# Performance work log

Hardware: AMD Instinct MI355X
Metric: run time of the kernel (lower is better)

Reference implementation:

```python
import jax, jax.numpy as jnp
import numpy as np

B = 1
F, Hh, Ww = 2, 30, 52           # grid_sizes (frames, height, width); 30*52 = 1560 tokens/frame
L = F * Hh * Ww                  # 3120 tokens
DIM = 1536
NH = 12
HD = DIM // NH                   # 128
EPS = 1e-6
SCALE = 1.0 / np.sqrt(HD)


def _rope_angles():
    # Matches causal_rope_apply: head_dim/2 = 64 complex channels split 22/21/21 (t/h/w).
    c = HD // 2
    tc = c - 2 * (c // 3)
    hc = c // 3
    wc = c // 3
    def ax(n, dh):
        inv = 1.0 / np.power(10000.0, np.arange(dh) * 2.0 / (2 * dh))
        return np.outer(np.arange(n), inv)  # [n, dh]
    ft, fh, fw = ax(F, tc), ax(Hh, hc), ax(Ww, wc)
    ang = np.concatenate([
        np.broadcast_to(ft[:, None, None, :], (F, Hh, Ww, tc)),
        np.broadcast_to(fh[None, :, None, :], (F, Hh, Ww, hc)),
        np.broadcast_to(fw[None, None, :, :], (F, Hh, Ww, wc)),
    ], axis=-1).reshape(L, c)
    return jnp.asarray(np.cos(ang), jnp.float32), jnp.asarray(np.sin(ang), jnp.float32)


def setup_inputs() -> dict:
    key = jax.random.key(0)
    ks = jax.random.split(key, 8)
    s = 1.0 / np.sqrt(DIM)
    d = {
        'x':  jax.random.normal(ks[0], (B, L, DIM), jnp.float32),
        'wq': jax.random.normal(ks[1], (DIM, DIM), jnp.float32) * s,
        'wk': jax.random.normal(ks[2], (DIM, DIM), jnp.float32) * s,
        'wv': jax.random.normal(ks[3], (DIM, DIM), jnp.float32) * s,
        'wo': jax.random.normal(ks[4], (DIM, DIM), jnp.float32) * s,
        'bq': jax.random.normal(ks[5], (DIM,), jnp.float32) * 0.02,
        'bk': jax.random.normal(ks[6], (DIM,), jnp.float32) * 0.02,
        'bv': jax.random.normal(ks[7], (DIM,), jnp.float32) * 0.02,
        'bo': jnp.zeros((DIM,), jnp.float32),
        'gq': jnp.ones((DIM,), jnp.float32),   # RMSNorm gain for q
        'gk': jnp.ones((DIM,), jnp.float32),   # RMSNorm gain for k
    }
    cos, sin = _rope_angles()
    d['freqs_cos'] = cos   # [L, HD//2]
    d['freqs_sin'] = sin
    return d


def _rms(x, g):
    return x * jax.lax.rsqrt(jnp.mean(x * x, axis=-1, keepdims=True) + EPS) * g


def _rope(x, cos, sin):
    # x: [B, L, NH, HD]; complex pairs are (even, odd) consecutive channels
    xs = x.reshape(B, L, NH, HD // 2, 2)
    xr, xi = xs[..., 0], xs[..., 1]
    c = cos[None, :, None, :]
    s = sin[None, :, None, :]
    out = jnp.stack([xr * c - xi * s, xr * s + xi * c], axis=-1)
    return out.reshape(B, L, NH, HD)


def reference(x, wq, wk, wv, wo, bq, bk, bv, bo, gq, gk, freqs_cos, freqs_sin):
    q = _rms(x @ wq + bq, gq).reshape(B, L, NH, HD)
    k = _rms(x @ wk + bk, gk).reshape(B, L, NH, HD)
    v = (x @ wv + bv).reshape(B, L, NH, HD)
    q = _rope(q, freqs_cos, freqs_sin)
    k = _rope(k, freqs_cos, freqs_sin)
    # block-causal per frame: query in frame i attends to keys in frames <= i
    frame = jnp.arange(L) // (Hh * Ww)
    mask = frame[None, :] <= frame[:, None]                     # [Lq, Lk]
    scores = jnp.einsum('bihd,bjhd->bhij', q, k) * SCALE        # [B, NH, L, L]
    scores = jnp.where(mask[None, None], scores, jnp.finfo(scores.dtype).min)
    p = jax.nn.softmax(scores, axis=-1)
    out = jnp.einsum('bhij,bjhd->bihd', p, v).reshape(B, L, DIM)
    return out @ wo + bo
```

## Files before the change

### kernel.cpp

```cpp
#include <hip/hip_runtime.h>
#include <hip/hip_bf16.h>

#define L_SEQ 3120
#define LPAD  3200
#define DIMN  1536
#define FRAME 1560
#define NHH   12
#define HDIM  128

using bh8   = __attribute__((ext_vector_type(8))) short;
using bh4   = __attribute__((ext_vector_type(4))) short;
using f32x4 = __attribute__((ext_vector_type(4))) float;
typedef unsigned short u16;
typedef unsigned int   u32;

static __device__ __forceinline__ u16 f2bf(float f) {
  __hip_bfloat16 h = __float2bfloat16(f);
  return *reinterpret_cast<u16*>(&h);
}
static __device__ __forceinline__ void gld16(const u16* g, u16* l) {
  __builtin_amdgcn_global_load_lds((const __attribute__((address_space(1))) void*)g,
                                   (__attribute__((address_space(3))) void*)l, 16, 0, 0);
}

__global__ __launch_bounds__(256) void prep_x_kern(const float* __restrict__ x,
                                                   u16* __restrict__ xb) {
  int i = (blockIdx.x * 256 + threadIdx.x) * 8;
  bh8 o;
  if (i < L_SEQ * DIMN) {
    float4 a = *(const float4*)&x[i];
    float4 b = *(const float4*)&x[i + 4];
    o[0] = (short)f2bf(a.x); o[1] = (short)f2bf(a.y);
    o[2] = (short)f2bf(a.z); o[3] = (short)f2bf(a.w);
    o[4] = (short)f2bf(b.x); o[5] = (short)f2bf(b.y);
    o[6] = (short)f2bf(b.z); o[7] = (short)f2bf(b.w);
  } else {
    o = (bh8){0, 0, 0, 0, 0, 0, 0, 0};
  }
  *(bh8*)&xb[i] = o;
}

__global__ __launch_bounds__(256) void transpose_w_kern(const float* __restrict__ w0, const float* __restrict__ w1,
                                 const float* __restrict__ w2, const float* __restrict__ w3,
                                 u16* __restrict__ t0, u16* __restrict__ t1,
                                 u16* __restrict__ t2, u16* __restrict__ t3) {
  __shared__ float tile[32][33];
  const float* src; u16* dst;
  switch (blockIdx.z) {
    case 0:  src = w0; dst = t0; break;
    case 1:  src = w1; dst = t1; break;
    case 2:  src = w2; dst = t2; break;
    default: src = w3; dst = t3; break;
  }
  int k0 = blockIdx.x * 32, n0 = blockIdx.y * 32;
  int tx = threadIdx.x, ty = threadIdx.y;
  #pragma unroll
  for (int i = 0; i < 4; i++)
    tile[ty * 4 + i][tx] = src[(size_t)(k0 + ty * 4 + i) * DIMN + n0 + tx];
  __syncthreads();
  #pragma unroll
  for (int i = 0; i < 4; i++) {
    int ry = ty * 4 + i;
    dst[(size_t)(n0 + ry) * DIMN + k0 + tx] = f2bf(tile[tx][ry]);
  }
}

__global__ __launch_bounds__(256) void zero_tail_kern(u16* __restrict__ ob) {
  int i = (blockIdx.x * 256 + threadIdx.x) * 8;
  *(bh8*)&ob[L_SEQ * DIMN + i] = (bh8){0, 0, 0, 0, 0, 0, 0, 0};
}

__global__ __launch_bounds__(256) void gemm_qkv(const u16* __restrict__ A,
                                                const u16* __restrict__ Bt,
                                                const float* __restrict__ bq,
                                                const float* __restrict__ bk,
                                                const float* __restrict__ bv,
                                                float* __restrict__ lin,
                                                u16* __restrict__ Vt) {
  __shared__ __align__(16) u16 Al[128 * 64];
  __shared__ __align__(16) u16 Bl[128 * 64];
  int t = threadIdx.x, lane = t & 63, w = t >> 6;
  int m0 = blockIdx.x * 128, n0 = blockIdx.y * 128;
  int wr = (w >> 1) * 64, wc = (w & 1) * 64;
  int r16 = lane & 15, g8 = (lane >> 4) * 8;
  int lrow = lane >> 3, lcol = (lane & 7) * 8;
  f32x4 acc[4][4];
  #pragma unroll
  for (int i = 0; i < 4; i++)
    #pragma unroll
    for (int j = 0; j < 4; j++) acc[i][j] = (f32x4){0.f, 0.f, 0.f, 0.f};

  const u16* Abase = A + (size_t)(m0 + w * 32 + lrow) * DIMN + lcol;
  const u16* Bbase = Bt + (size_t)(n0 + w * 32 + lrow) * DIMN + lcol;

  for (int kt = 0; kt < DIMN; kt += 64) {
    __syncthreads();
    #pragma unroll
    for (int j = 0; j < 4; j++) {
      gld16(Abase + (size_t)j * 8 * DIMN + kt, &Al[(w * 32 + j * 8) * 64]);
      gld16(Bbase + (size_t)j * 8 * DIMN + kt, &Bl[(w * 32 + j * 8) * 64]);
    }
    __syncthreads();
    bh8 af[2][4], bf[2][4];
    #pragma unroll
    for (int kk = 0; kk < 2; kk++) {
      #pragma unroll
      for (int i = 0; i < 4; i++)
        af[kk][i] = *(const bh8*)&Al[(wr + i * 16 + r16) * 64 + kk * 32 + g8];
      #pragma unroll
      for (int j = 0; j < 4; j++)
        bf[kk][j] = *(const bh8*)&Bl[(wc + j * 16 + r16) * 64 + kk * 32 + g8];
    }
    #pragma unroll
    for (int kk = 0; kk < 2; kk++)
      #pragma unroll
      for (int i = 0; i < 4; i++)
        #pragma unroll
        for (int j = 0; j < 4; j++)
          acc[i][j] = __builtin_amdgcn_mfma_f32_16x16x32_bf16(af[kk][i], bf[kk][j], acc[i][j], 0, 0, 0);
  }

  int cr = (lane >> 4) * 4, cc = lane & 15;
  int seg = n0 / DIMN;
  int nb0 = n0 - seg * DIMN;
  const float* bp = (seg == 0) ? bq : (seg == 1) ? bk : bv;
  if (seg < 2) {
    #pragma unroll
    for (int j = 0; j < 4; j++) {
      int n = nb0 + wc + j * 16 + cc;
      float bvv = bp[n];
      #pragma unroll
      for (int i = 0; i < 4; i++) {
        int m = m0 + wr + i * 16 + cr;
        float* orow = lin + (size_t)m * (2 * DIMN) + seg * DIMN + n;
        #pragma unroll
        for (int r = 0; r < 4; r++) orow[(size_t)r * (2 * DIMN)] = acc[i][j][r] + bvv;
      }
    }
  } else {
    #pragma unroll
    for (int j = 0; j < 4; j++) {
      int d = nb0 + wc + j * 16 + cc;
      float bvv = bp[d];
      #pragma unroll
      for (int i = 0; i < 4; i++) {
        int m = m0 + wr + i * 16 + cr;
        if (m < L_SEQ) {
          bh4 o;
          #pragma unroll
          for (int r = 0; r < 4; r++) o[r] = (short)f2bf(acc[i][j][r] + bvv);
          *(bh4*)&Vt[(size_t)d * L_SEQ + m] = o;
        }
      }
    }
  }
}

__global__ __launch_bounds__(256) void gemm_out(const u16* __restrict__ A,
                                                const u16* __restrict__ Bt,
                                                const float* __restrict__ bias,
                                                float* __restrict__ out) {
  __shared__ __align__(16) u16 Al[128 * 64];
  __shared__ __align__(16) u16 Bl[128 * 64];
  int t = threadIdx.x, lane = t & 63, w = t >> 6;
  int m0 = blockIdx.x * 128, n0 = blockIdx.y * 128;
  int wr = (w >> 1) * 64, wc = (w & 1) * 64;
  int r16 = lane & 15, g8 = (lane >> 4) * 8;
  int lrow = lane >> 3, lcol = (lane & 7) * 8;
  f32x4 acc[4][4];
  #pragma unroll
  for (int i = 0; i < 4; i++)
    #pragma unroll
    for (int j = 0; j < 4; j++) acc[i][j] = (f32x4){0.f, 0.f, 0.f, 0.f};

  const u16* Abase = A + (size_t)(m0 + w * 32 + lrow) * DIMN + lcol;
  const u16* Bbase = Bt + (size_t)(n0 + w * 32 + lrow) * DIMN + lcol;

  for (int kt = 0; kt < DIMN; kt += 64) {
    __syncthreads();
    #pragma unroll
    for (int j = 0; j < 4; j++) {
      gld16(Abase + (size_t)j * 8 * DIMN + kt, &Al[(w * 32 + j * 8) * 64]);
      gld16(Bbase + (size_t)j * 8 * DIMN + kt, &Bl[(w * 32 + j * 8) * 64]);
    }
    __syncthreads();
    bh8 af[2][4], bf[2][4];
    #pragma unroll
    for (int kk = 0; kk < 2; kk++) {
      #pragma unroll
      for (int i = 0; i < 4; i++)
        af[kk][i] = *(const bh8*)&Al[(wr + i * 16 + r16) * 64 + kk * 32 + g8];
      #pragma unroll
      for (int j = 0; j < 4; j++)
        bf[kk][j] = *(const bh8*)&Bl[(wc + j * 16 + r16) * 64 + kk * 32 + g8];
    }
    #pragma unroll
    for (int kk = 0; kk < 2; kk++)
      #pragma unroll
      for (int i = 0; i < 4; i++)
        #pragma unroll
        for (int j = 0; j < 4; j++)
          acc[i][j] = __builtin_amdgcn_mfma_f32_16x16x32_bf16(af[kk][i], bf[kk][j], acc[i][j], 0, 0, 0);
  }

  int cr = (lane >> 4) * 4, cc = lane & 15;
  #pragma unroll
  for (int j = 0; j < 4; j++) {
    int n = n0 + wc + j * 16 + cc;
    float bvv = bias[n];
    #pragma unroll
    for (int i = 0; i < 4; i++) {
      int m = m0 + wr + i * 16 + cr;
      if (m < L_SEQ) {
        #pragma unroll
        for (int r = 0; r < 4; r++) out[(size_t)(m + r) * DIMN + n] = acc[i][j][r] + bvv;
      }
    }
  }
}

__global__ __launch_bounds__(256) void postproc_qk(const float* __restrict__ lin,
                                                   const float* __restrict__ gq,
                                                   const float* __restrict__ gk,
                                                   const float* __restrict__ fc,
                                                   const float* __restrict__ fs,
                                                   u16* __restrict__ Qb, u16* __restrict__ Kb) {
  int l = blockIdx.x, t = threadIdx.x;
  int lane = t & 63, w = t >> 6;
  const float2* qr = (const float2*)(lin + (size_t)l * (2 * DIMN));
  const float2* kr = qr + DIMN / 2;
  float2 qv[3], kv[3];
  float ssq = 0.f, ssk = 0.f;
  #pragma unroll
  for (int j = 0; j < 3; j++) {
    qv[j] = qr[t + j * 256];
    kv[j] = kr[t + j * 256];
    ssq += qv[j].x * qv[j].x + qv[j].y * qv[j].y;
    ssk += kv[j].x * kv[j].x + kv[j].y * kv[j].y;
  }
  __shared__ float red[8];
  #pragma unroll
  for (int off = 32; off; off >>= 1) {
    ssq += __shfl_xor(ssq, off);
    ssk += __shfl_xor(ssk, off);
  }
  if (lane == 0) { red[w] = ssq; red[4 + w] = ssk; }
  __syncthreads();
  float rrq = rsqrtf((red[0] + red[1] + red[2] + red[3]) * (1.0f / DIMN) + 1e-6f);
  float rrk = rsqrtf((red[4] + red[5] + red[6] + red[7]) * (1.0f / DIMN) + 1e-6f);
  u32* qo = (u32*)Qb;
  u32* ko = (u32*)Kb;
  #pragma unroll
  for (int j = 0; j < 3; j++) {
    int p = t + j * 256;
    int head = p >> 6, c = p & 63;
    float co = fc[l * 64 + c], si = fs[l * 64 + c];
    float2 g2, o;
    size_t idx = ((size_t)head * L_SEQ + l) * 64 + c;
    g2 = ((const float2*)gq)[p];
    o.x = qv[j].x * rrq * g2.x; o.y = qv[j].y * rrq * g2.y;
    qo[idx] = (u32)f2bf(o.x * co - o.y * si) | ((u32)f2bf(o.x * si + o.y * co) << 16);
    g2 = ((const float2*)gk)[p];
    o.x = kv[j].x * rrk * g2.x; o.y = kv[j].y * rrk * g2.y;
    ko[idx] = (u32)f2bf(o.x * co - o.y * si) | ((u32)f2bf(o.x * si + o.y * co) << 16);
  }
}

__global__ __launch_bounds__(256) void attn_kern(const u16* __restrict__ Q,
                                                 const u16* __restrict__ K,
                                                 const u16* __restrict__ Vt,
                                                 u16* __restrict__ Ob) {
  __shared__ __align__(16) u16 KlB[2][64 * 128];
  __shared__ __align__(16) u16 VlB[2][128 * 64];
  __shared__ __align__(16) u16 Pl[4][16 * 72];
  int t = threadIdx.x, lane = t & 63, w = t >> 6;
  int h = blockIdx.y;
  int bx = 48 - blockIdx.x;
  int qb = bx * 64, qr0 = qb + w * 16;
  int r16 = lane & 15, grp = lane >> 4, g8 = grp * 8;
  int cr = grp * 4, cc = lane & 15;
  const float sl = 0.08838834764831845f * 1.4426950408889634f;

  int qld = qr0 + r16; if (qld > L_SEQ - 1) qld = L_SEQ - 1;
  const u16* qrow = Q + ((size_t)h * L_SEQ + qld) * HDIM;
  bh8 qf[4];
  #pragma unroll
  for (int kk = 0; kk < 4; kk++) qf[kk] = *(const bh8*)&qrow[kk * 32 + g8];

  const u16* Kbase = K + (size_t)h * L_SEQ * HDIM;
  const u16* Vbase = Vt + (size_t)h * HDIM * L_SEQ;

  float m_run[4] = {-3.0e38f, -3.0e38f, -3.0e38f, -3.0e38f};
  float l_part[4] = {0.f, 0.f, 0.f, 0.f};
  f32x4 accO[8];
  #pragma unroll
  for (int i = 0; i < 8; i++) accO[i] = (f32x4){0.f, 0.f, 0.f, 0.f};

  int klim_min = (qr0 < FRAME) ? FRAME : L_SEQ;
  int klimr[4];
  #pragma unroll
  for (int r = 0; r < 4; r++) klimr[r] = (qr0 + cr + r < FRAME) ? FRAME : L_SEQ;
  int klimB = (qb + 63 < FRAME) ? FRAME : L_SEQ;
  int nkt = (klimB + 63) >> 6;

  auto stage = [&](int buf, int it) {
    int kt = it << 6;
    #pragma unroll
    for (int j = 0; j < 4; j++) {
      int rr = w * 16 + j * 4 + (lane >> 4);
      int grow = kt + rr; grow = (grow > L_SEQ - 1) ? L_SEQ - 1 : grow;
      int gc = ((lane & 15) ^ (rr & 7)) * 8;
      gld16(Kbase + (size_t)grow * HDIM + gc, &KlB[buf][(w * 16 + j * 4) * 128]);
    }
    #pragma unroll
    for (int j = 0; j < 4; j++) {
      int vr = w * 32 + j * 8 + (lane >> 3);
      int gc = kt + ((lane & 7) ^ (vr & 7)) * 8;
      gc = (gc > L_SEQ - 8) ? L_SEQ - 8 : gc;
      gld16(Vbase + (size_t)vr * L_SEQ + gc, &VlB[buf][(w * 32 + j * 8) * 64]);
    }
  };

  stage(0, 0);
  for (int it = 0; it < nkt; ++it) {
    int buf = it & 1, kt = it << 6;
    if (it + 1 < nkt) {
      stage(buf ^ 1, it + 1);
      asm volatile("s_waitcnt vmcnt(8)" ::: "memory");
    } else {
      asm volatile("s_waitcnt vmcnt(0)" ::: "memory");
    }
    __builtin_amdgcn_s_barrier();
    __builtin_amdgcn_sched_barrier(0);

    f32x4 s[4];
    #pragma unroll
    for (int sb = 0; sb < 4; sb++) s[sb] = (f32x4){0.f, 0.f, 0.f, 0.f};
    #pragma unroll
    for (int kk = 0; kk < 4; kk++)
      #pragma unroll
      for (int sb = 0; sb < 4; sb++) {
        int rr = sb * 16 + r16;
        bh8 kf = *(const bh8*)&KlB[buf][rr * 128 + (((kk * 4 + grp) ^ (rr & 7)) * 8)];
        s[sb] = __builtin_amdgcn_mfma_f32_16x16x32_bf16(qf[kk], kf, s[sb], 0, 0, 0);
      }

    float v[4][4];
    if (kt + 64 > klim_min) {
      #pragma unroll
      for (int sb = 0; sb < 4; sb++) {
        int j = kt + sb * 16 + cc;
        #pragma unroll
        for (int r = 0; r < 4; r++) v[sb][r] = (j < klimr[r]) ? s[sb][r] * sl : -3.0e38f;
      }
    } else {
      #pragma unroll
      for (int sb = 0; sb < 4; sb++)
        #pragma unroll
        for (int r = 0; r < 4; r++) v[sb][r] = s[sb][r] * sl;
    }

    float loc[4];
    #pragma unroll
    for (int r = 0; r < 4; r++)
      loc[r] = fmaxf(fmaxf(v[0][r], v[1][r]), fmaxf(v[2][r], v[3][r]));
    bool need = (loc[0] > m_run[0] + 8.f) || (loc[1] > m_run[1] + 8.f) ||
                (loc[2] > m_run[2] + 8.f) || (loc[3] > m_run[3] + 8.f);
    if (__any((int)need)) {
      float facs[4];
      #pragma unroll
      for (int r = 0; r < 4; r++) {
        float mx = loc[r];
        mx = fmaxf(mx, __shfl_xor(mx, 1));
        mx = fmaxf(mx, __shfl_xor(mx, 2));
        mx = fmaxf(mx, __shfl_xor(mx, 4));
        mx = fmaxf(mx, __shfl_xor(mx, 8));
        float mnew = fmaxf(m_run[r], mx);
        facs[r] = exp2f(m_run[r] - mnew);
        m_run[r] = mnew;
        l_part[r] *= facs[r];
      }
      #pragma unroll
      for (int nb = 0; nb < 8; nb++)
        #pragma unroll
        for (int r = 0; r < 4; r++) accO[nb][r] *= facs[r];
    }
    #pragma unroll
    for (int sb = 0; sb < 4; sb++)
      #pragma unroll
      for (int r = 0; r < 4; r++) {
        float p = exp2f(v[sb][r] - m_run[r]);
        l_part[r] += p;
        Pl[w][(cr + r) * 72 + sb * 16 + cc] = f2bf(p);
      }

    bh8 pf0 = *(const bh8*)&Pl[w][r16 * 72 + g8];
    bh8 pf1 = *(const bh8*)&Pl[w][r16 * 72 + 32 + g8];
    #pragma unroll
    for (int nb = 0; nb < 8; nb++) {
      int vrow = nb * 16 + r16;
      bh8 vf0 = *(const bh8*)&VlB[buf][vrow * 64 + ((grp ^ (vrow & 7)) * 8)];
      bh8 vf1 = *(const bh8*)&VlB[buf][vrow * 64 + (((4 + grp) ^ (vrow & 7)) * 8)];
      accO[nb] = __builtin_amdgcn_mfma_f32_16x16x32_bf16(pf0, vf0, accO[nb], 0, 0, 0);
      accO[nb] = __builtin_amdgcn_mfma_f32_16x16x32_bf16(pf1, vf1, accO[nb], 0, 0, 0);
    }
    __builtin_amdgcn_s_barrier();
  }

  #pragma unroll
  for (int r = 0; r < 4; r++) {
    float lr = l_part[r];
    lr += __shfl_xor(lr, 1);
    lr += __shfl_xor(lr, 2);
    lr += __shfl_xor(lr, 4);
    lr += __shfl_xor(lr, 8);
    l_part[r] = 1.0f / lr;
  }
  #pragma unroll
  for (int nb = 0; nb < 8; nb++)
    #pragma unroll
    for (int r = 0; r < 4; r++) {
      int qi = qr0 + cr + r;
      if (qi < L_SEQ)
        Ob[(size_t)qi * DIMN + h * HDIM + nb * 16 + cc] = f2bf(accO[nb][r] * l_part[r]);
    }
}

extern "C" void kernel_launch(void* const* d_in, const int* in_sizes, int n_in,
                              void* d_out, int out_size, void* d_ws, size_t ws_size,
                              hipStream_t stream) {
  const float* x  = (const float*)d_in[0];
  const float* wq = (const float*)d_in[1];
  const float* wk = (const float*)d_in[2];
  const float* wv = (const float*)d_in[3];
  const float* wo = (const float*)d_in[4];
  const float* bq = (const float*)d_in[5];
  const float* bk = (const float*)d_in[6];
  const float* bv = (const float*)d_in[7];
  const float* bo = (const float*)d_in[8];
  const float* gq = (const float*)d_in[9];
  const float* gk = (const float*)d_in[10];
  const float* fc = (const float*)d_in[11];
  const float* fs = (const float*)d_in[12];

  char* ws = (char*)d_ws;
  u16* xb   = (u16*)(ws);
  u16* Btq  = (u16*)(ws + 9830400);
  u16* wot  = (u16*)(ws + 23986176);
  u16* Qb   = (u16*)(ws + 28704768);
  u16* Kb   = (u16*)(ws + 38289408);
  u16* Vt   = (u16*)(ws + 47874048);
  u16* Ob   = (u16*)(ws + 57458688);
  float* lin = (float*)(ws + 67289088);

  prep_x_kern<<<2400, 256, 0, stream>>>(x, xb);
  transpose_w_kern<<<dim3(48, 48, 4), dim3(32, 8), 0, stream>>>(
      wq, wk, wv, wo, Btq, Btq + DIMN * DIMN, Btq + 2 * DIMN * DIMN, wot);
  zero_tail_kern<<<60, 256, 0, stream>>>(Ob);

  gemm_qkv<<<dim3(25, 36), 256, 0, stream>>>(xb, Btq, bq, bk, bv, lin, Vt);
  postproc_qk<<<L_SEQ, 256, 0, stream>>>(lin, gq, gk, fc, fs, Qb, Kb);
  attn_kern<<<dim3(49, 12), 256, 0, stream>>>(Qb, Kb, Vt, Ob);
  gemm_out<<<dim3(25, 12), 256, 0, stream>>>(Ob, wot, bo, (float*)d_out);
}
```

Before: 398.2 us.

## Process two 16-row query slices per wave in attention to double K/V reuse

Each attention wave now handles 32 query rows (two 16-row slices), making the block tile 128 queries and halving the grid. Every K/V tile loaded into LDS and every K fragment read is reused for twice as many queries, reducing memory traffic and LDS reads per FLOP. Priority hints are added around the MFMA sections. The trade-off is higher register usage, lower occupancy and a smaller grid with coarser causal-tile granularity.

```diff
diff --git a/kernel.cpp b/kernel.cpp
--- a/kernel.cpp
+++ b/kernel.cpp
@@ -275,32 +275,42 @@
   __shared__ __align__(16) u16 Pl[4][16 * 72];
   int t = threadIdx.x, lane = t & 63, w = t >> 6;
   int h = blockIdx.y;
-  int bx = 48 - blockIdx.x;
-  int qb = bx * 64, qr0 = qb + w * 16;
+  int bx = 24 - blockIdx.x;
+  int qb = bx * 128, qr0 = qb + w * 32;
   int r16 = lane & 15, grp = lane >> 4, g8 = grp * 8;
   int cr = grp * 4, cc = lane & 15;
   const float sl = 0.08838834764831845f * 1.4426950408889634f;
 
-  int qld = qr0 + r16; if (qld > L_SEQ - 1) qld = L_SEQ - 1;
-  const u16* qrow = Q + ((size_t)h * L_SEQ + qld) * HDIM;
-  bh8 qf[4];
-  #pragma unroll
-  for (int kk = 0; kk < 4; kk++) qf[kk] = *(const bh8*)&qrow[kk * 32 + g8];
+  bh8 qf[2][4];
+  #pragma unroll
+  for (int qs = 0; qs < 2; qs++) {
+    int qld = qr0 + qs * 16 + r16; if (qld > L_SEQ - 1) qld = L_SEQ - 1;
+    const u16* qrow = Q + ((size_t)h * L_SEQ + qld) * HDIM;
+    #pragma unroll
+    for (int kk = 0; kk < 4; kk++) qf[qs][kk] = *(const bh8*)&qrow[kk * 32 + g8];
+  }
 
   const u16* Kbase = K + (size_t)h * L_SEQ * HDIM;
   const u16* Vbase = Vt + (size_t)h * HDIM * L_SEQ;
 
-  float m_run[4] = {-3.0e38f, -3.0e38f, -3.0e38f, -3.0e38f};
-  float l_part[4] = {0.f, 0.f, 0.f, 0.f};
-  f32x4 accO[8];
-  #pragma unroll
-  for (int i = 0; i < 8; i++) accO[i] = (f32x4){0.f, 0.f, 0.f, 0.f};
+  float m_run[2][4], l_part[2][4];
+  f32x4 accO[2][8];
+  #pragma unroll
+  for (int qs = 0; qs < 2; qs++) {
+    #pragma unroll
+    for (int r = 0; r < 4; r++) { m_run[qs][r] = -3.0e38f; l_part[qs][r] = 0.f; }
+    #pragma unroll
+    for (int i = 0; i < 8; i++) accO[qs][i] = (f32x4){0.f, 0.f, 0.f, 0.f};
+  }
 
   int klim_min = (qr0 < FRAME) ? FRAME : L_SEQ;
-  int klimr[4];
-  #pragma unroll
-  for (int r = 0; r < 4; r++) klimr[r] = (qr0 + cr + r < FRAME) ? FRAME : L_SEQ;
-  int klimB = (qb + 63 < FRAME) ? FRAME : L_SEQ;
+  int klimr[2][4];
+  #pragma unroll
+  for (int qs = 0; qs < 2; qs++)
+    #pragma unroll
+    for (int r = 0; r < 4; r++)
+      klimr[qs][r] = (qr0 + qs * 16 + cr + r < FRAME) ? FRAME : L_SEQ;
+  int klimB = (qb + 127 < FRAME) ? FRAME : L_SEQ;
   int nkt = (klimB + 63) >> 6;
 
   auto stage = [&](int buf, int it) {
@@ -333,97 +343,125 @@
     __builtin_amdgcn_s_barrier();
     __builtin_amdgcn_sched_barrier(0);
 
-    f32x4 s[4];
-    #pragma unroll
-    for (int sb = 0; sb < 4; sb++) s[sb] = (f32x4){0.f, 0.f, 0.f, 0.f};
-    #pragma unroll
-    for (int kk = 0; kk < 4; kk++)
-      #pragma unroll
-      for (int sb = 0; sb < 4; sb++) {
-        int rr = sb * 16 + r16;
-        bh8 kf = *(const bh8*)&KlB[buf][rr * 128 + (((kk * 4 + grp) ^ (rr & 7)) * 8)];
-        s[sb] = __builtin_amdgcn_mfma_f32_16x16x32_bf16(qf[kk], kf, s[sb], 0, 0, 0);
-      }
-
-    float v[4][4];
+    f32x4 s[2][4];
+    #pragma unroll
+    for (int qs = 0; qs < 2; qs++)
+      #pragma unroll
+      for (int sb = 0; sb < 4; sb++) s[qs][sb] = (f32x4){0.f, 0.f, 0.f, 0.f};
+    #pragma unroll
+    for (int sb = 0; sb < 4; sb++) {
+      int rr = sb * 16 + r16;
+      bh8 kf[4];
+      #pragma unroll
+      for (int kk = 0; kk < 4; kk++)
+        kf[kk] = *(const bh8*)&KlB[buf][rr * 128 + (((kk * 4 + grp) ^ (rr & 7)) * 8)];
+      __builtin_amdgcn_s_setprio(1);
+      #pragma unroll
+      for (int qs = 0; qs < 2; qs++)
+        #pragma unroll
+        for (int kk = 0; kk < 4; kk++)
+          s[qs][sb] = __builtin_amdgcn_mfma_f32_16x16x32_bf16(qf[qs][kk], kf[kk], s[qs][sb], 0, 0, 0);
+      __builtin_amdgcn_s_setprio(0);
+    }
+
+    float v[2][4][4];
     if (kt + 64 > klim_min) {
       #pragma unroll
-      for (int sb = 0; sb < 4; sb++) {
-        int j = kt + sb * 16 + cc;
-        #pragma unroll
-        for (int r = 0; r < 4; r++) v[sb][r] = (j < klimr[r]) ? s[sb][r] * sl : -3.0e38f;
-      }
+      for (int qs = 0; qs < 2; qs++)
+        #pragma unroll
+        for (int sb = 0; sb < 4; sb++) {
+          int j = kt + sb * 16 + cc;
+          #pragma unroll
+          for (int r = 0; r < 4; r++)
+            v[qs][sb][r] = (j < klimr[qs][r]) ? s[qs][sb][r] * sl : -3.0e38f;
+        }
     } else {
       #pragma unroll
+      for (int qs = 0; qs < 2; qs++)
+        #pragma unroll
+        for (int sb = 0; sb < 4; sb++)
+          #pragma unroll
+          for (int r = 0; r < 4; r++) v[qs][sb][r] = s[qs][sb][r] * sl;
+    }
+
+    float loc[2][4];
+    bool need = false;
+    #pragma unroll
+    for (int qs = 0; qs < 2; qs++)
+      #pragma unroll
+      for (int r = 0; r < 4; r++) {
+        loc[qs][r] = fmaxf(fmaxf(v[qs][0][r], v[qs][1][r]), fmaxf(v[qs][2][r], v[qs][3][r]));
+        need = need || (loc[qs][r] > m_run[qs][r] + 8.f);
+      }
+    if (__any((int)need)) {
+      #pragma unroll
+      for (int qs = 0; qs < 2; qs++) {
+        float facs[4];
+        #pragma unroll
+        for (int r = 0; r < 4; r++) {
+          float mx = loc[qs][r];
+          mx = fmaxf(mx, __shfl_xor(mx, 1));
+          mx = fmaxf(mx, __shfl_xor(mx, 2));
+          mx = fmaxf(mx, __shfl_xor(mx, 4));
+          mx = fmaxf(mx, __shfl_xor(mx, 8));
+          float mnew = fmaxf(m_run[qs][r], mx);
+          facs[r] = exp2f(m_run[qs][r] - mnew);
+          m_run[qs][r] = mnew;
+          l_part[qs][r] *= facs[r];
+        }
+        #pragma unroll
+        for (int nb = 0; nb < 8; nb++)
+          #pragma unroll
+          for (int r = 0; r < 4; r++) accO[qs][nb][r] *= facs[r];
+      }
+    }
+
+    #pragma unroll
+    for (int qs = 0; qs < 2; qs++) {
+      #pragma unroll
       for (int sb = 0; sb < 4; sb++)
         #pragma unroll
-        for (int r = 0; r < 4; r++) v[sb][r] = s[sb][r] * sl;
-    }
-
-    float loc[4];
-    #pragma unroll
-    for (int r = 0; r < 4; r++)
-      loc[r] = fmaxf(fmaxf(v[0][r], v[1][r]), fmaxf(v[2][r], v[3][r]));
-    bool need = (loc[0] > m_run[0] + 8.f) || (loc[1] > m_run[1] + 8.f) ||
-                (loc[2] > m_run[2] + 8.f) || (loc[3] > m_run[3] + 8.f);
-    if (__any((int)need)) {
-      float facs[4];
+        for (int r = 0; r < 4; r++) {
+          float p = exp2f(v[qs][sb][r] - m_run[qs][r]);
+          l_part[qs][r] += p;
+          Pl[w][(cr + r) * 72 + sb * 16 + cc] = f2bf(p);
+        }
+      bh8 pf0 = *(const bh8*)&Pl[w][r16 * 72 + g8];
+      bh8 pf1 = *(const bh8*)&Pl[w][r16 * 72 + 32 + g8];
+      __builtin_amdgcn_s_setprio(1);
+      #pragma unroll
+      for (int nb = 0; nb < 8; nb++) {
+        int vrow = nb * 16 + r16;
+        bh8 vf0 = *(const bh8*)&VlB[buf][vrow * 64 + ((grp ^ (vrow & 7)) * 8)];
+        bh8 vf1 = *(const bh8*)&VlB[buf][vrow * 64 + (((4 + grp) ^ (vrow & 7)) * 8)];
+        accO[qs][nb] = __builtin_amdgcn_mfma_f32_16x16x32_bf16(pf0, vf0, accO[qs][nb], 0, 0, 0);
+        accO[qs][nb] = __builtin_amdgcn_mfma_f32_16x16x32_bf16(pf1, vf1, accO[qs][nb], 0, 0, 0);
+      }
+      __builtin_amdgcn_s_setprio(0);
+    }
+    __builtin_amdgcn_s_barrier();
+  }
+
+  #pragma unroll
+  for (int qs = 0; qs < 2; qs++) {
+    #pragma unroll
+    for (int r = 0; r < 4; r++) {
+      float lr = l_part[qs][r];
+      lr += __shfl_xor(lr, 1);
+      lr += __shfl_xor(lr, 2);
+      lr += __shfl_xor(lr, 4);
+      lr += __shfl_xor(lr, 8);
+      l_part[qs][r] = 1.0f / lr;
+    }
+    #pragma unroll
+    for (int nb = 0; nb < 8; nb++)
       #pragma unroll
       for (int r = 0; r < 4; r++) {
-        float mx = loc[r];
-        mx = fmaxf(mx, __shfl_xor(mx, 1));
-        mx = fmaxf(mx, __shfl_xor(mx, 2));
-        mx = fmaxf(mx, __shfl_xor(mx, 4));
-        mx = fmaxf(mx, __shfl_xor(mx, 8));
-        float mnew = fmaxf(m_run[r], mx);
-        facs[r] = exp2f(m_run[r] - mnew);
-        m_run[r] = mnew;
-        l_part[r] *= facs[r];
-      }
-      #pragma unroll
-      for (int nb = 0; nb < 8; nb++)
-        #pragma unroll
-        for (int r = 0; r < 4; r++) accO[nb][r] *= facs[r];
-    }
-    #pragma unroll
-    for (int sb = 0; sb < 4; sb++)
-      #pragma unroll
-      for (int r = 0; r < 4; r++) {
-        float p = exp2f(v[sb][r] - m_run[r]);
-        l_part[r] += p;
-        Pl[w][(cr + r) * 72 + sb * 16 + cc] = f2bf(p);
-      }
-
-    bh8 pf0 = *(const bh8*)&Pl[w][r16 * 72 + g8];
-    bh8 pf1 = *(const bh8*)&Pl[w][r16 * 72 + 32 + g8];
-    #pragma unroll
-    for (int nb = 0; nb < 8; nb++) {
-      int vrow = nb * 16 + r16;
-      bh8 vf0 = *(const bh8*)&VlB[buf][vrow * 64 + ((grp ^ (vrow & 7)) * 8)];
-      bh8 vf1 = *(const bh8*)&VlB[buf][vrow * 64 + (((4 + grp) ^ (vrow & 7)) * 8)];
-      accO[nb] = __builtin_amdgcn_mfma_f32_16x16x32_bf16(pf0, vf0, accO[nb], 0, 0, 0);
-      accO[nb] = __builtin_amdgcn_mfma_f32_16x16x32_bf16(pf1, vf1, accO[nb], 0, 0, 0);
-    }
-    __builtin_amdgcn_s_barrier();
-  }
-
-  #pragma unroll
-  for (int r = 0; r < 4; r++) {
-    float lr = l_part[r];
-    lr += __shfl_xor(lr, 1);
-    lr += __shfl_xor(lr, 2);
-    lr += __shfl_xor(lr, 4);
-    lr += __shfl_xor(lr, 8);
-    l_part[r] = 1.0f / lr;
-  }
-  #pragma unroll
-  for (int nb = 0; nb < 8; nb++)
-    #pragma unroll
-    for (int r = 0; r < 4; r++) {
-      int qi = qr0 + cr + r;
-      if (qi < L_SEQ)
-        Ob[(size_t)qi * DIMN + h * HDIM + nb * 16 + cc] = f2bf(accO[nb][r] * l_part[r]);
-    }
+        int qi = qr0 + qs * 16 + cr + r;
+        if (qi < L_SEQ)
+          Ob[(size_t)qi * DIMN + h * HDIM + nb * 16 + cc] = f2bf(accO[qs][nb][r] * l_part[qs][r]);
+      }
+  }
 }
 
 extern "C" void kernel_launch(void* const* d_in, const int* in_sizes, int n_in,
@@ -460,6 +498,6 @@
 
   gemm_qkv<<<dim3(25, 36), 256, 0, stream>>>(xb, Btq, bq, bk, bv, lin, Vt);
   postproc_qk<<<L_SEQ, 256, 0, stream>>>(lin, gq, gk, fc, fs, Qb, Kb);
-  attn_kern<<<dim3(49, 12), 256, 0, stream>>>(Qb, Kb, Vt, Ob);
+  attn_kern<<<dim3(25, 12), 256, 0, stream>>>(Qb, Kb, Vt, Ob);
   gemm_out<<<dim3(25, 12), 256, 0, stream>>>(Ob, wot, bo, (float*)d_out);
 }
```

Result: slower. 467.6 us (+17.4%).

## Load V fragments straight to registers and remap attention blocks across XCDs

Applied to the files above, without the earlier changes.

The attention kernel no longer stages V tiles in LDS. Each wave now reads its V fragments directly from global memory into registers at the start of every key tile, which frees LDS and removes the trailing per-iteration barrier. The grid becomes 1D, with a block-to-(head, q-tile) mapping meant to group consecutive work on each XCD for L2 locality. It also raises occupancy through launch bounds and adds s_setprio around the MFMA bursts. The risks are strided, less-coalesced global V loads, the V loads on the final tile running past the row end, and the loss of the heavy-tiles-first ordering.

```diff
diff --git a/kernel.cpp b/kernel.cpp
--- a/kernel.cpp
+++ b/kernel.cpp
@@ -266,16 +266,17 @@
   }
 }
 
-__global__ __launch_bounds__(256) void attn_kern(const u16* __restrict__ Q,
-                                                 const u16* __restrict__ K,
-                                                 const u16* __restrict__ Vt,
-                                                 u16* __restrict__ Ob) {
+__global__ __launch_bounds__(256, 3) void attn_kern(const u16* __restrict__ Q,
+                                                    const u16* __restrict__ K,
+                                                    const u16* __restrict__ Vt,
+                                                    u16* __restrict__ Ob) {
   __shared__ __align__(16) u16 KlB[2][64 * 128];
-  __shared__ __align__(16) u16 VlB[2][128 * 64];
   __shared__ __align__(16) u16 Pl[4][16 * 72];
   int t = threadIdx.x, lane = t & 63, w = t >> 6;
-  int h = blockIdx.y;
-  int bx = 48 - blockIdx.x;
+  int id = blockIdx.x;
+  int xcd = id & 7, sub = id >> 3;
+  int g = (xcd < 4) ? (xcd * 74 + sub) : (296 + (xcd - 4) * 73 + sub);
+  int h = g / 49, bx = g - h * 49;
   int qb = bx * 64, qr0 = qb + w * 16;
   int r16 = lane & 15, grp = lane >> 4, g8 = grp * 8;
   int cr = grp * 4, cc = lane & 15;
@@ -303,47 +304,50 @@
   int klimB = (qb + 63 < FRAME) ? FRAME : L_SEQ;
   int nkt = (klimB + 63) >> 6;
 
-  auto stage = [&](int buf, int it) {
+  auto stageK = [&](int buf, int it) {
     int kt = it << 6;
     #pragma unroll
     for (int j = 0; j < 4; j++) {
       int rr = w * 16 + j * 4 + (lane >> 4);
-      int grow = kt + rr; grow = (grow > L_SEQ - 1) ? L_SEQ - 1 : grow;
+      int grow = kt + rr; if (grow > L_SEQ - 1) grow = L_SEQ - 1;
       int gc = ((lane & 15) ^ (rr & 7)) * 8;
       gld16(Kbase + (size_t)grow * HDIM + gc, &KlB[buf][(w * 16 + j * 4) * 128]);
     }
-    #pragma unroll
-    for (int j = 0; j < 4; j++) {
-      int vr = w * 32 + j * 8 + (lane >> 3);
-      int gc = kt + ((lane & 7) ^ (vr & 7)) * 8;
-      gc = (gc > L_SEQ - 8) ? L_SEQ - 8 : gc;
-      gld16(Vbase + (size_t)vr * L_SEQ + gc, &VlB[buf][(w * 32 + j * 8) * 64]);
-    }
   };
 
-  stage(0, 0);
+  stageK(0, 0);
   for (int it = 0; it < nkt; ++it) {
     int buf = it & 1, kt = it << 6;
-    if (it + 1 < nkt) {
-      stage(buf ^ 1, it + 1);
-      asm volatile("s_waitcnt vmcnt(8)" ::: "memory");
-    } else {
-      asm volatile("s_waitcnt vmcnt(0)" ::: "memory");
-    }
+    asm volatile("s_waitcnt vmcnt(0)" ::: "memory");
     __builtin_amdgcn_s_barrier();
     __builtin_amdgcn_sched_barrier(0);
 
+    bh8 vfr[16];
+    #pragma unroll
+    for (int nb = 0; nb < 8; nb++) {
+      int vrow = nb * 16 + r16;
+      const u16* vp = Vbase + (size_t)vrow * L_SEQ + kt;
+      vfr[2 * nb]     = *(const bh8*)&vp[g8];
+      vfr[2 * nb + 1] = *(const bh8*)&vp[32 + g8];
+    }
+    if (it + 1 < nkt) stageK(buf ^ 1, it + 1);
+
     f32x4 s[4];
     #pragma unroll
     for (int sb = 0; sb < 4; sb++) s[sb] = (f32x4){0.f, 0.f, 0.f, 0.f};
     #pragma unroll
-    for (int kk = 0; kk < 4; kk++)
-      #pragma unroll
-      for (int sb = 0; sb < 4; sb++) {
-        int rr = sb * 16 + r16;
-        bh8 kf = *(const bh8*)&KlB[buf][rr * 128 + (((kk * 4 + grp) ^ (rr & 7)) * 8)];
-        s[sb] = __builtin_amdgcn_mfma_f32_16x16x32_bf16(qf[kk], kf, s[sb], 0, 0, 0);
-      }
+    for (int sb = 0; sb < 4; sb++) {
+      int rr = sb * 16 + r16;
+      bh8 kf[4];
+      #pragma unroll
+      for (int kk = 0; kk < 4; kk++)
+        kf[kk] = *(const bh8*)&KlB[buf][rr * 128 + (((kk * 4 + grp) ^ (rr & 7)) * 8)];
+      __builtin_amdgcn_s_setprio(1);
+      #pragma unroll
+      for (int kk = 0; kk < 4; kk++)
+        s[sb] = __builtin_amdgcn_mfma_f32_16x16x32_bf16(qf[kk], kf[kk], s[sb], 0, 0, 0);
+      __builtin_amdgcn_s_setprio(0);
+    }
 
     float v[4][4];
     if (kt + 64 > klim_min) {
@@ -396,15 +400,13 @@
 
     bh8 pf0 = *(const bh8*)&Pl[w][r16 * 72 + g8];
     bh8 pf1 = *(const bh8*)&Pl[w][r16 * 72 + 32 + g8];
+    __builtin_amdgcn_s_setprio(1);
     #pragma unroll
     for (int nb = 0; nb < 8; nb++) {
-      int vrow = nb * 16 + r16;
-      bh8 vf0 = *(const bh8*)&VlB[buf][vrow * 64 + ((grp ^ (vrow & 7)) * 8)];
-      bh8 vf1 = *(const bh8*)&VlB[buf][vrow * 64 + (((4 + grp) ^ (vrow & 7)) * 8)];
-      accO[nb] = __builtin_amdgcn_mfma_f32_16x16x32_bf16(pf0, vf0, accO[nb], 0, 0, 0);
-      accO[nb] = __builtin_amdgcn_mfma_f32_16x16x32_bf16(pf1, vf1, accO[nb], 0, 0, 0);
-    }
-    __builtin_amdgcn_s_barrier();
+      accO[nb] = __builtin_amdgcn_mfma_f32_16x16x32_bf16(pf0, vfr[2 * nb],     accO[nb], 0, 0, 0);
+      accO[nb] = __builtin_amdgcn_mfma_f32_16x16x32_bf16(pf1, vfr[2 * nb + 1], accO[nb], 0, 0, 0);
+    }
+    __builtin_amdgcn_s_setprio(0);
   }
 
   #pragma unroll
@@ -460,6 +462,6 @@
 
   gemm_qkv<<<dim3(25, 36), 256, 0, stream>>>(xb, Btq, bq, bk, bv, lin, Vt);
   postproc_qk<<<L_SEQ, 256, 0, stream>>>(lin, gq, gk, fc, fs, Qb, Kb);
-  attn_kern<<<dim3(49, 12), 256, 0, stream>>>(Qb, Kb, Vt, Ob);
+  attn_kern<<<588, 256, 0, stream>>>(Qb, Kb, Vt, Ob);
   gemm_out<<<dim3(25, 12), 256, 0, stream>>>(Ob, wot, bo, (float*)d_out);
 }
```

New measurement: 532.6 us. 33.8% more time.
